# Kernel optimization log

Hardware: AMD Instinct MI355X
Metric: run time of the kernel (lower is better)

The kernel has to match this reference:

```python
import jax, jax.numpy as jnp
import numpy as np

HIDDEN = 768
HEADS = 12
HEAD_DIM = HIDDEN // HEADS
DEPTH = 8
B, S = 4, 512


def setup_inputs() -> dict:
    key = jax.random.key(0)
    ks = jax.random.split(key, 12)
    sc = 0.02
    return {
        "hidden_states": jax.random.normal(ks[0], (B, S, HIDDEN), dtype=jnp.float32),
        "attention_mask": jnp.ones((B, S), dtype=jnp.int32),
        "Wq": jax.random.normal(ks[1], (HIDDEN, HIDDEN), dtype=jnp.float32) * sc,
        "bq": jnp.zeros((HIDDEN,), dtype=jnp.float32),
        "Wk": jax.random.normal(ks[2], (HIDDEN, HIDDEN), dtype=jnp.float32) * sc,
        "bk": jnp.zeros((HIDDEN,), dtype=jnp.float32),
        "Wv": jax.random.normal(ks[3], (HIDDEN, HIDDEN), dtype=jnp.float32) * sc,
        "bv": jnp.zeros((HIDDEN,), dtype=jnp.float32),
        "Wqd": jax.random.normal(ks[4], (HIDDEN * DEPTH, HIDDEN), dtype=jnp.float32) * sc,
        "bqd": jnp.zeros((HIDDEN * DEPTH,), dtype=jnp.float32),
        "Wkd": jax.random.normal(ks[5], (HIDDEN * DEPTH, HIDDEN), dtype=jnp.float32) * sc,
        "bkd": jnp.zeros((HIDDEN * DEPTH,), dtype=jnp.float32),
    }


def reference(hidden_states, attention_mask, Wq, bq, Wk, bk, Wv, bv, Wqd, bqd, Wkd, bkd):
    b, s, _ = hidden_states.shape
    # projections (nn.Linear: x @ W.T + b)
    V = (hidden_states @ Wv.T + bv).reshape(b, s, HEADS, HEAD_DIM).transpose(0, 2, 1, 3)  # [B,H,S,hd]
    Qd = (hidden_states @ Wqd.T + bqd).reshape(b, s, HEADS, HEAD_DIM, DEPTH).transpose(0, 2, 1, 3, 4)  # [B,H,S,hd,D]
    Kd = (hidden_states @ Wkd.T + bkd).reshape(b, s, HEADS, HEAD_DIM, DEPTH).transpose(0, 2, 1, 3, 4)
    # per-depth QK^T scores: [B,H,Sq,Sk,D]
    scores = jnp.einsum('bhqed,bhked->bhqkd', Qd, Kd) / np.sqrt(HEAD_DIM).astype(np.float32)
    # mask broadcasts over the key axis: [B,1,1,S,1]
    mask = attention_mask[:, None, None, :, None]
    scores = jnp.where(mask == 0, jnp.float32(-1e9), scores)
    # softmax over key dim (axis=-2 of [B,H,Sq,Sk,D])
    weights = jax.nn.softmax(scores, axis=3)
    # per-depth AV matmul, stacked on leading depth axis: [D,B,H,S,hd]
    depth_outputs = jnp.einsum('bhqkd,bhke->dbhqe', weights, V)
    return depth_outputs
```

## Files before the change

kernel.cpp:

```cpp
#include <hip/hip_runtime.h>

#define HIDDEN 768
#define HEADS 12
#define HEAD_DIM 64
#define DEPTH 8
#define BB 4
#define SS 512
#define MM (BB * SS)
#define NQD (HIDDEN * DEPTH)

typedef __bf16 bf16x8 __attribute__((ext_vector_type(8)));
typedef float f32x4 __attribute__((ext_vector_type(4)));
typedef float f32x16 __attribute__((ext_vector_type(16)));
typedef unsigned short u16x8 __attribute__((ext_vector_type(8)));

static __device__ __forceinline__ unsigned short f2bf(float f) {
  union { float f; unsigned u; } c; c.f = f;
  unsigned u = c.u;
  u = u + 0x7fffu + ((u >> 16) & 1u);
  return (unsigned short)(u >> 16);
}

static __device__ __forceinline__ unsigned cvt_pk_bf16(float lo, float hi) {
  unsigned r;
  asm("v_cvt_pk_bf16_f32 %0, %1, %2" : "=v"(r) : "v"(lo), "v"(hi));
  return r;
}

static __device__ __forceinline__ void gld16(const void* g, void* l) {
  __builtin_amdgcn_global_load_lds((const __attribute__((address_space(1))) void*)g,
                                   (__attribute__((address_space(3))) void*)l, 16, 0, 0);
}

__global__ void convert2_f32_bf16(const float* __restrict__ s0, unsigned short* __restrict__ d0,
                                  int n4_0, const float* __restrict__ s1,
                                  unsigned short* __restrict__ d1, int n4_1) {
  int i = blockIdx.x * blockDim.x + threadIdx.x;
  const float* src; unsigned short* dst; int j;
  if (i < n4_0) { src = s0; dst = d0; j = i; }
  else { j = i - n4_0; if (j >= n4_1) return; src = s1; dst = d1; }
  float4 v = reinterpret_cast<const float4*>(src)[j];
  ushort4 o;
  o.x = f2bf(v.x); o.y = f2bf(v.y); o.z = f2bf(v.z); o.w = f2bf(v.w);
  reinterpret_cast<ushort4*>(dst)[j] = o;
}

__global__ void convert_w_perm2(const float* __restrict__ s0, const float* __restrict__ s1,
                                unsigned short* __restrict__ dst, int n4each) {
  int i = blockIdx.x * blockDim.x + threadIdx.x;
  const float* src = s0; unsigned short* d = dst; int j = i;
  if (i >= n4each) {
    j = i - n4each;
    if (j >= n4each) return;
    src = s1; d = dst + (size_t)NQD * HIDDEN;
  }
  int row = j / 192;
  int cg  = j - row * 192;
  int nr = (row & ~511) | ((row & 7) << 6) | ((row >> 3) & 63);
  float4 v = reinterpret_cast<const float4*>(src)[j];
  ushort4 o;
  o.x = f2bf(v.x); o.y = f2bf(v.y); o.z = f2bf(v.z); o.w = f2bf(v.w);
  reinterpret_cast<ushort4*>(&d[(size_t)nr * HIDDEN])[cg] = o;
}

__global__ void convert_bias_perm2(const float* __restrict__ s0, const float* __restrict__ s1,
                                   float* __restrict__ dst, int n) {
  int i = blockIdx.x * blockDim.x + threadIdx.x;
  const float* src = s0; float* d = dst; int j = i;
  if (i >= n) {
    j = i - n;
    if (j >= n) return;
    src = s1; d = dst + n;
  }
  int nr = (j & ~511) | ((j & 7) << 6) | ((j >> 3) & 63);
  d[nr] = src[j];
}

__global__ __launch_bounds__(256) void gemm_bt(
    const unsigned short* __restrict__ A, const unsigned short* __restrict__ W,
    const float* __restrict__ bias, unsigned short* __restrict__ out0, int K) {
  __shared__ unsigned short At[2][4096];
  __shared__ unsigned short Bt[2][4096];
  const int tid = threadIdx.x;
  const int nwg = gridDim.x * gridDim.y;
  const int orig = blockIdx.y * gridDim.x + blockIdx.x;
  const int wg = (orig & 7) * (nwg >> 3) + (orig >> 3);
  const int bm = (wg % gridDim.x) * 128;
  const int bn = (wg / gridDim.x) * 128;
  const int wave = tid >> 6, lane = tid & 63;
  const int wm = (wave >> 1) * 64, wn = (wave & 1) * 64;
  const int lg = lane >> 4, lr = lane & 15;
  const int srow = tid >> 2, scol = (tid & 3) * 8;
  f32x4 acc[4][4] = {};
  const unsigned short* aptr = A + (size_t)(bm + srow) * K + scol;
  const unsigned short* wptr = W + (size_t)(bn + srow) * K + scol;

  auto stage = [&](int buf, int k0) {
    gld16(aptr + k0,                  &At[buf][tid * 8]);
    gld16(aptr + (size_t)64 * K + k0, &At[buf][2048 + tid * 8]);
    gld16(wptr + k0,                  &Bt[buf][tid * 8]);
    gld16(wptr + (size_t)64 * K + k0, &Bt[buf][2048 + tid * 8]);
  };

  stage(0, 0);
  __syncthreads();

  int cur = 0;
  for (int k0 = 32; k0 <= K; k0 += 32) {
    if (k0 < K) stage(cur ^ 1, k0);
    bf16x8 af[4], bfr[4];
#pragma unroll
    for (int mi = 0; mi < 4; ++mi)
      af[mi] = *reinterpret_cast<const bf16x8*>(&At[cur][(wm + mi * 16 + lr) * 32 + lg * 8]);
#pragma unroll
    for (int ni = 0; ni < 4; ++ni)
      bfr[ni] = *reinterpret_cast<const bf16x8*>(&Bt[cur][(wn + ni * 16 + lr) * 32 + lg * 8]);
#pragma unroll
    for (int mi = 0; mi < 4; ++mi)
#pragma unroll
      for (int ni = 0; ni < 4; ++ni)
        acc[mi][ni] = __builtin_amdgcn_mfma_f32_16x16x32_bf16(af[mi], bfr[ni], acc[mi][ni], 0, 0, 0);
    __syncthreads();
    cur ^= 1;
  }

#pragma unroll
  for (int mi = 0; mi < 4; ++mi)
#pragma unroll
    for (int ni = 0; ni < 4; ++ni)
#pragma unroll
      for (int i = 0; i < 4; ++i) {
        int m = bm + wm + mi * 16 + lg * 4 + i;
        int n = bn + wn + ni * 16 + lr;
        float v = acc[mi][ni][i] + bias[m];
        size_t addr = ((size_t)((n >> 9) * 12 + (m >> 6)) * 64 + (size_t)(m & 63)) * 512 + (size_t)(n & 511);
        out0[addr] = f2bf(v);
      }
}

__global__ __launch_bounds__(512, 2) void gemm_qk256(
    const unsigned short* __restrict__ A, const unsigned short* __restrict__ W,
    const float* __restrict__ bias, unsigned short* __restrict__ out0,
    unsigned short* __restrict__ out1, int K) {
  __shared__ unsigned short At[2][8192];
  __shared__ unsigned short Bt[2][6144];
  const int tid = threadIdx.x;
  const int nwg = gridDim.x * gridDim.y;
  const int orig = blockIdx.y * gridDim.x + blockIdx.x;
  const int wg = (orig & 7) * (nwg >> 3) + (orig >> 3);
  const int bm = (wg % gridDim.x) * 256;
  const int bn = (wg / gridDim.x) * 192;
  const int wave = tid >> 6, lane = tid & 63;
  const int wr = wave >> 2, wc = wave & 3;
  const int lg = lane >> 4, lr = lane & 15;

  const int rA0 = tid >> 2,           cA0 = (tid & 3) << 3;
  const int rA1 = (tid + 512) >> 2;
  const bool hasB1 = tid < 256;
  const int rB1 = (tid + 512) >> 2;
  const int dA0 = rA0 * 64 + ((cA0 << 1) ^ (((rA0 >> 1) & 3) << 4));
  const int dA1 = rA1 * 64 + ((cA0 << 1) ^ (((rA1 >> 1) & 3) << 4));
  const int dB0 = dA0;
  const int dB1 = rB1 * 64 + ((cA0 << 1) ^ (((rB1 >> 1) & 3) << 4));
  const unsigned short* pA0 = A + (size_t)(bm + rA0) * K + cA0;
  const unsigned short* pA1 = A + (size_t)(bm + rA1) * K + cA0;
  const unsigned short* pB0 = W + (size_t)(bn + rA0) * K + cA0;
  const unsigned short* pB1 = W + (size_t)(bn + rB1) * K + cA0;

  u16x8 a0A = {}, a1A = {}, b0A = {}, b1A = {};
  u16x8 a0B = {}, a1B = {}, b0B = {}, b1B = {};

  auto gloadA = [&](int k0) {
    a0A = *reinterpret_cast<const u16x8*>(pA0 + k0);
    a1A = *reinterpret_cast<const u16x8*>(pA1 + k0);
    b0A = *reinterpret_cast<const u16x8*>(pB0 + k0);
    if (hasB1) b1A = *reinterpret_cast<const u16x8*>(pB1 + k0);
  };
  auto gloadB = [&](int k0) {
    a0B = *reinterpret_cast<const u16x8*>(pA0 + k0);
    a1B = *reinterpret_cast<const u16x8*>(pA1 + k0);
    b0B = *reinterpret_cast<const u16x8*>(pB0 + k0);
    if (hasB1) b1B = *reinterpret_cast<const u16x8*>(pB1 + k0);
  };
  auto lwriteA = [&](int buf) {
    *reinterpret_cast<u16x8*>((char*)At[buf] + dA0) = a0A;
    *reinterpret_cast<u16x8*>((char*)At[buf] + dA1) = a1A;
    *reinterpret_cast<u16x8*>((char*)Bt[buf] + dB0) = b0A;
    if (hasB1) *reinterpret_cast<u16x8*>((char*)Bt[buf] + dB1) = b1A;
  };
  auto lwriteB = [&](int buf) {
    *reinterpret_cast<u16x8*>((char*)At[buf] + dA0) = a0B;
    *reinterpret_cast<u16x8*>((char*)At[buf] + dA1) = a1B;
    *reinterpret_cast<u16x8*>((char*)Bt[buf] + dB0) = b0B;
    if (hasB1) *reinterpret_cast<u16x8*>((char*)Bt[buf] + dB1) = b1B;
  };

  const int rdswz = ((((lr >> 1) & 3) ^ lg) << 4);

  f32x4 acc[8][3] = {};
  auto compute = [&](int buf) {
    bf16x8 af[8], bfr[3];
    const char* abase = (const char*)At[buf];
    const char* bbase = (const char*)Bt[buf];
#pragma unroll
    for (int mi = 0; mi < 8; ++mi) {
      const int row = wr * 128 + mi * 16 + lr;
      af[mi] = *reinterpret_cast<const bf16x8*>(abase + row * 64 + rdswz);
    }
#pragma unroll
    for (int ni = 0; ni < 3; ++ni) {
      const int row = wc * 48 + ni * 16 + lr;
      bfr[ni] = *reinterpret_cast<const bf16x8*>(bbase + row * 64 + rdswz);
    }
#pragma unroll
    for (int mi = 0; mi < 8; ++mi)
#pragma unroll
      for (int ni = 0; ni < 3; ++ni)
        acc[mi][ni] = __builtin_amdgcn_mfma_f32_16x16x32_bf16(af[mi], bfr[ni], acc[mi][ni], 0, 0, 0);
  };

  const int NT = K / 32;
  gloadA(0);
  gloadB(32);
  lwriteA(0);
  __syncthreads();

  for (int tt = 0; tt < NT; tt += 2) {
    if (tt + 2 < NT) gloadA((tt + 2) * 32);
    compute(0);
    if (tt + 1 < NT) lwriteB(1);
    __syncthreads();
    if (tt + 1 < NT) {
      if (tt + 3 < NT) gloadB((tt + 3) * 32);
      compute(1);
      if (tt + 2 < NT) lwriteA(0);
      __syncthreads();
    }
  }

  unsigned short* outp = out0;
  int nbase = 0;
  float scale = 0.125f;
  if (bn >= NQD) { outp = out1; nbase = NQD; scale = 1.0f; }
#pragma unroll
  for (int mi = 0; mi < 8; ++mi)
#pragma unroll
    for (int ni = 0; ni < 3; ++ni)
#pragma unroll
      for (int i = 0; i < 4; ++i) {
        int m = bm + wr * 128 + mi * 16 + lg * 4 + i;
        int n = bn + wc * 48 + ni * 16 + lr;
        float v = (acc[mi][ni][i] + bias[n]) * scale;
        int nr = n - nbase;
        size_t addr = ((size_t)(((m >> 9) * 12 + (nr >> 9)) * 8 + ((nr >> 6) & 7)) * 512 + (size_t)(m & 511)) * 64 + (size_t)(nr & 63);
        outp[addr] = f2bf(v);
      }
}

__global__ __launch_bounds__(256) void attn32(
    const unsigned short* __restrict__ Qd, const unsigned short* __restrict__ Kd,
    const unsigned short* __restrict__ Vt, const int* __restrict__ mask,
    float* __restrict__ out) {
  __shared__ unsigned char KsB[64 * 128];
  __shared__ unsigned char VsB[64 * 128];
  __shared__ float mLds[64];
  __shared__ int mflag;
  const int tid = threadIdx.x;
  const int bid = blockIdx.x;
  const int qt = bid & 3;
  const int inst = bid >> 2;
  const int bh = inst >> 3;
  const int b = bh / 12;
  const int wave = tid >> 6, lane = tid & 63;
  const int l31 = lane & 31, hi = lane >> 5;
  const size_t qkbase = (size_t)inst * (SS * 64);
  const size_t vbase = (size_t)bh * (64 * SS);

  if (tid == 0) mflag = 0;
  __syncthreads();
  {
    int m0 = mask[b * SS + tid], m1 = mask[b * SS + 256 + tid];
    if ((m0 == 0) || (m1 == 0)) mflag = 1;
  }
  __syncthreads();
  const bool hasmask = (mflag != 0);

  const int q0w = qt * 128 + wave * 32;
  bf16x8 aq[4];
  {
    const unsigned short* qrow = Qd + qkbase + (size_t)(q0w + l31) * 64 + 8 * hi;
#pragma unroll
    for (int s = 0; s < 4; ++s)
      aq[s] = *reinterpret_cast<const bf16x8*>(qrow + 16 * s);
  }

  const int sr = tid >> 3;
  const int sc = (tid & 7) * 8;
  const int swz_lo = sr * 128 + ((sc * 2) ^ ((sr & 7) << 4));
  const int swz_hi = (sr + 32) * 128 + ((sc * 2) ^ (((sr + 32) & 7) << 4));

  f32x16 o[2] = {};
  float psum = 0.f;

  u16x8 rk0 = *reinterpret_cast<const u16x8*>(&Kd[qkbase + (size_t)sr * 64 + sc]);
  u16x8 rk1 = *reinterpret_cast<const u16x8*>(&Kd[qkbase + (size_t)(sr + 32) * 64 + sc]);
  u16x8 rv0 = *reinterpret_cast<const u16x8*>(&Vt[vbase + (size_t)sr * SS + sc]);
  u16x8 rv1 = *reinterpret_cast<const u16x8*>(&Vt[vbase + (size_t)(sr + 32) * SS + sc]);

  for (int t = 0; t < SS / 64; ++t) {
    *reinterpret_cast<u16x8*>(KsB + swz_lo) = rk0;
    *reinterpret_cast<u16x8*>(KsB + swz_hi) = rk1;
    *reinterpret_cast<u16x8*>(VsB + swz_lo) = rv0;
    *reinterpret_cast<u16x8*>(VsB + swz_hi) = rv1;
    if (hasmask && tid < 64) mLds[tid] = mask[b * SS + t * 64 + tid] ? 0.f : -1e9f;
    __syncthreads();

    if (t < SS / 64 - 1) {
      const int kn = (t + 1) * 64;
      rk0 = *reinterpret_cast<const u16x8*>(&Kd[qkbase + (size_t)(kn + sr) * 64 + sc]);
      rk1 = *reinterpret_cast<const u16x8*>(&Kd[qkbase + (size_t)(kn + sr + 32) * 64 + sc]);
      rv0 = *reinterpret_cast<const u16x8*>(&Vt[vbase + (size_t)sr * SS + kn + sc]);
      rv1 = *reinterpret_cast<const u16x8*>(&Vt[vbase + (size_t)(sr + 32) * SS + kn + sc]);
    }

    f32x16 st[2];
    __builtin_amdgcn_s_setprio(1);
#pragma unroll
    for (int kh = 0; kh < 2; ++kh) {
      f32x16 acc = {};
      const int row = kh * 32 + l31;
      const int rswz = (row & 7) << 4;
#pragma unroll
      for (int s = 0; s < 4; ++s) {
        bf16x8 ak = *reinterpret_cast<const bf16x8*>(KsB + row * 128 + ((32 * s + 16 * hi) ^ rswz));
        acc = __builtin_amdgcn_mfma_f32_32x32x16_bf16(ak, aq[s], acc, 0, 0, 0);
      }
      st[kh] = acc;
    }
    __builtin_amdgcn_s_setprio(0);

    if (hasmask) {
#pragma unroll
      for (int h = 0; h < 2; ++h)
#pragma unroll
        for (int r = 0; r < 16; ++r)
          st[h][r] += mLds[32 * h + (r & 3) + 8 * (r >> 2) + 4 * hi];
    }

    float pv[2][16];
#pragma unroll
    for (int h = 0; h < 2; ++h)
#pragma unroll
      for (int r = 0; r < 16; ++r) {
        float p = __expf(st[h][r]);
        psum += p;
        pv[h][r] = p;
      }

    __builtin_amdgcn_s_setprio(1);
#pragma unroll
    for (int ks = 0; ks < 4; ++ks) {
      const int h = ks >> 1, rb = 8 * (ks & 1);
      unsigned w0 = cvt_pk_bf16(pv[h][rb + 0], pv[h][rb + 1]);
      unsigned w1 = cvt_pk_bf16(pv[h][rb + 2], pv[h][rb + 3]);
      unsigned w2 = cvt_pk_bf16(pv[h][rb + 4], pv[h][rb + 5]);
      unsigned w3 = cvt_pk_bf16(pv[h][rb + 6], pv[h][rb + 7]);
      asm("v_permlane32_swap_b32 %0, %1" : "+v"(w0), "+v"(w2));
      asm("v_permlane32_swap_b32 %0, %1" : "+v"(w1), "+v"(w3));
      union { unsigned u[4]; bf16x8 v; } pa;
      pa.u[0] = w0; pa.u[1] = w1; pa.u[2] = w2; pa.u[3] = w3;
#pragma unroll
      for (int et = 0; et < 2; ++et) {
        const int vrow = 32 * et + l31;
        bf16x8 bv = *reinterpret_cast<const bf16x8*>(
            VsB + vrow * 128 + ((32 * ks + 16 * hi) ^ ((vrow & 7) << 4)));
        o[et] = __builtin_amdgcn_mfma_f32_32x32x16_bf16(pa.v, bv, o[et], 0, 0, 0);
      }
    }
    __builtin_amdgcn_s_setprio(0);
    __syncthreads();
  }

  psum += __shfl_xor(psum, 32);
  float inv = 1.f / psum;
  float iv[16];
#pragma unroll
  for (int r = 0; r < 16; ++r)
    iv[r] = __shfl(inv, (r & 3) + 8 * (r >> 2) + 4 * hi);

  const int d = inst & 7;
  const int hh = bh % 12;
  const size_t obase = (((size_t)d * BB + b) * HEADS + hh) * (SS * 64);
#pragma unroll
  for (int et = 0; et < 2; ++et)
#pragma unroll
    for (int r = 0; r < 16; ++r) {
      const int qrow = (r & 3) + 8 * (r >> 2) + 4 * hi;
      out[obase + (size_t)(q0w + qrow) * 64 + 32 * et + l31] = o[et][r] * iv[r];
    }
}

extern "C" void kernel_launch(void* const* d_in, const int* in_sizes, int n_in,
                              void* d_out, int out_size, void* d_ws, size_t ws_size,
                              hipStream_t stream) {
  const float* hs  = (const float*)d_in[0];
  const int* mask  = (const int*)d_in[1];
  const float* Wv  = (const float*)d_in[6];
  const float* bv  = (const float*)d_in[7];
  const float* Wqd = (const float*)d_in[8];
  const float* bqd = (const float*)d_in[9];
  const float* Wkd = (const float*)d_in[10];
  const float* bkd = (const float*)d_in[11];

  char* ws = (char*)d_ws;
  unsigned short* A_bf   = (unsigned short*)ws; ws += (size_t)MM * HIDDEN * 2;
  unsigned short* Wv_bf  = (unsigned short*)ws; ws += (size_t)HIDDEN * HIDDEN * 2;
  unsigned short* Wqk_bf = (unsigned short*)ws; ws += (size_t)(2 * NQD) * HIDDEN * 2;
  float*          bqk_p  = (float*)ws;          ws += (size_t)(2 * NQD) * 4;
  unsigned short* Qd     = (unsigned short*)ws; ws += (size_t)MM * NQD * 2;
  unsigned short* Kd     = (unsigned short*)ws; ws += (size_t)MM * NQD * 2;
  unsigned short* Vt     = (unsigned short*)ws; ws += (size_t)MM * HIDDEN * 2;

  {
    int a4 = MM * HIDDEN / 4, b4 = HIDDEN * HIDDEN / 4;
    convert2_f32_bf16<<<(a4 + b4 + 255) / 256, 256, 0, stream>>>(hs, A_bf, a4, Wv, Wv_bf, b4);
  }
  {
    int n4 = NQD * HIDDEN / 4;
    convert_w_perm2<<<(2 * n4 + 255) / 256, 256, 0, stream>>>(Wqd, Wkd, Wqk_bf, n4);
    convert_bias_perm2<<<(2 * NQD + 255) / 256, 256, 0, stream>>>(bqd, bkd, bqk_p, NQD);
  }

  gemm_bt<<<dim3(HIDDEN / 128, MM / 128), 256, 0, stream>>>(
      Wv_bf, A_bf, bv, Vt, HIDDEN);
  gemm_qk256<<<dim3(MM / 256, 2 * NQD / 192), 512, 0, stream>>>(
      A_bf, Wqk_bf, bqk_p, Qd, Kd, HIDDEN);

  attn32<<<BB * HEADS * DEPTH * (SS / 128), 256, 0, stream>>>(Qd, Kd, Vt, mask, (float*)d_out);
}
```

Measured before the change: 132.1 us.

## Split attention key range across two wave groups with LDS reduction

The attention kernel grows from 256 to 512 threads. Two groups of four waves each process half of the key sequence for the same query tile, each with its own K/V LDS buffers. At the end, group 1 writes its partial outputs and row sums to shared memory and group 0 adds them before normalizing and storing. The aim is more parallelism and latency hiding per block, paid for with a shared-memory reduction, extra LDS use and possibly lower occupancy.

```diff
diff --git a/kernel.cpp b/kernel.cpp
--- a/kernel.cpp
+++ b/kernel.cpp
@@ -257,13 +257,12 @@
       }
 }
 
-__global__ __launch_bounds__(256) void attn32(
+__global__ __launch_bounds__(512) void attn32(
     const unsigned short* __restrict__ Qd, const unsigned short* __restrict__ Kd,
     const unsigned short* __restrict__ Vt, const int* __restrict__ mask,
     float* __restrict__ out) {
-  __shared__ unsigned char KsB[64 * 128];
-  __shared__ unsigned char VsB[64 * 128];
-  __shared__ float mLds[64];
+  __shared__ __align__(16) char smem[32768 + 512];
+  __shared__ float psbuf[4][64];
   __shared__ int mflag;
   const int tid = threadIdx.x;
   const int bid = blockIdx.x;
@@ -272,20 +271,21 @@
   const int bh = inst >> 3;
   const int b = bh / 12;
   const int wave = tid >> 6, lane = tid & 63;
+  const int grp = wave >> 2, w4 = wave & 3;
   const int l31 = lane & 31, hi = lane >> 5;
   const size_t qkbase = (size_t)inst * (SS * 64);
   const size_t vbase = (size_t)bh * (64 * SS);
+  unsigned char* KsB = (unsigned char*)smem + grp * 8192;
+  unsigned char* VsB = (unsigned char*)smem + 16384 + grp * 8192;
+  float* mLds = (float*)(smem + 32768) + grp * 64;
 
   if (tid == 0) mflag = 0;
   __syncthreads();
-  {
-    int m0 = mask[b * SS + tid], m1 = mask[b * SS + 256 + tid];
-    if ((m0 == 0) || (m1 == 0)) mflag = 1;
-  }
+  if (mask[b * SS + tid] == 0) mflag = 1;
   __syncthreads();
   const bool hasmask = (mflag != 0);
 
-  const int q0w = qt * 128 + wave * 32;
+  const int q0w = qt * 128 + w4 * 32;
   bf16x8 aq[4];
   {
     const unsigned short* qrow = Qd + qkbase + (size_t)(q0w + l31) * 64 + 8 * hi;
@@ -294,29 +294,31 @@
       aq[s] = *reinterpret_cast<const bf16x8*>(qrow + 16 * s);
   }
 
-  const int sr = tid >> 3;
-  const int sc = (tid & 7) * 8;
+  const int t256 = tid & 255;
+  const int sr = t256 >> 3;
+  const int sc = (t256 & 7) * 8;
   const int swz_lo = sr * 128 + ((sc * 2) ^ ((sr & 7) << 4));
   const int swz_hi = (sr + 32) * 128 + ((sc * 2) ^ (((sr + 32) & 7) << 4));
+  const int kg = grp * 256;
 
   f32x16 o[2] = {};
   float psum = 0.f;
 
-  u16x8 rk0 = *reinterpret_cast<const u16x8*>(&Kd[qkbase + (size_t)sr * 64 + sc]);
-  u16x8 rk1 = *reinterpret_cast<const u16x8*>(&Kd[qkbase + (size_t)(sr + 32) * 64 + sc]);
-  u16x8 rv0 = *reinterpret_cast<const u16x8*>(&Vt[vbase + (size_t)sr * SS + sc]);
-  u16x8 rv1 = *reinterpret_cast<const u16x8*>(&Vt[vbase + (size_t)(sr + 32) * SS + sc]);
-
-  for (int t = 0; t < SS / 64; ++t) {
+  u16x8 rk0 = *reinterpret_cast<const u16x8*>(&Kd[qkbase + (size_t)(kg + sr) * 64 + sc]);
+  u16x8 rk1 = *reinterpret_cast<const u16x8*>(&Kd[qkbase + (size_t)(kg + sr + 32) * 64 + sc]);
+  u16x8 rv0 = *reinterpret_cast<const u16x8*>(&Vt[vbase + (size_t)sr * SS + kg + sc]);
+  u16x8 rv1 = *reinterpret_cast<const u16x8*>(&Vt[vbase + (size_t)(sr + 32) * SS + kg + sc]);
+
+  for (int t = 0; t < 4; ++t) {
     *reinterpret_cast<u16x8*>(KsB + swz_lo) = rk0;
     *reinterpret_cast<u16x8*>(KsB + swz_hi) = rk1;
     *reinterpret_cast<u16x8*>(VsB + swz_lo) = rv0;
     *reinterpret_cast<u16x8*>(VsB + swz_hi) = rv1;
-    if (hasmask && tid < 64) mLds[tid] = mask[b * SS + t * 64 + tid] ? 0.f : -1e9f;
+    if (hasmask && t256 < 64) mLds[t256] = mask[b * SS + kg + t * 64 + t256] ? 0.f : -1e9f;
     __syncthreads();
 
-    if (t < SS / 64 - 1) {
-      const int kn = (t + 1) * 64;
+    if (t < 3) {
+      const int kn = kg + (t + 1) * 64;
       rk0 = *reinterpret_cast<const u16x8*>(&Kd[qkbase + (size_t)(kn + sr) * 64 + sc]);
       rk1 = *reinterpret_cast<const u16x8*>(&Kd[qkbase + (size_t)(kn + sr + 32) * 64 + sc]);
       rv0 = *reinterpret_cast<const u16x8*>(&Vt[vbase + (size_t)sr * SS + kn + sc]);
@@ -381,23 +383,41 @@
     __syncthreads();
   }
 
-  psum += __shfl_xor(psum, 32);
-  float inv = 1.f / psum;
-  float iv[16];
-#pragma unroll
-  for (int r = 0; r < 16; ++r)
-    iv[r] = __shfl(inv, (r & 3) + 8 * (r >> 2) + 4 * hi);
-
-  const int d = inst & 7;
-  const int hh = bh % 12;
-  const size_t obase = (((size_t)d * BB + b) * HEADS + hh) * (SS * 64);
-#pragma unroll
-  for (int et = 0; et < 2; ++et)
-#pragma unroll
-    for (int r = 0; r < 16; ++r) {
-      const int qrow = (r & 3) + 8 * (r >> 2) + 4 * hi;
-      out[obase + (size_t)(q0w + qrow) * 64 + 32 * et + l31] = o[et][r] * iv[r];
-    }
+  float* cbuf = (float*)smem;
+  if (grp == 1) {
+#pragma unroll
+    for (int et = 0; et < 2; ++et)
+#pragma unroll
+      for (int r = 0; r < 16; ++r)
+        cbuf[(et * 16 + r) * 256 + w4 * 64 + lane] = o[et][r];
+    psbuf[w4][lane] = psum;
+  }
+  __syncthreads();
+  if (grp == 0) {
+#pragma unroll
+    for (int et = 0; et < 2; ++et)
+#pragma unroll
+      for (int r = 0; r < 16; ++r)
+        o[et][r] += cbuf[(et * 16 + r) * 256 + w4 * 64 + lane];
+    psum += psbuf[w4][lane];
+    psum += __shfl_xor(psum, 32);
+    float inv = 1.f / psum;
+    float iv[16];
+#pragma unroll
+    for (int r = 0; r < 16; ++r)
+      iv[r] = __shfl(inv, (r & 3) + 8 * (r >> 2) + 4 * hi);
+
+    const int d = inst & 7;
+    const int hh = bh % 12;
+    const size_t obase = (((size_t)d * BB + b) * HEADS + hh) * (SS * 64);
+#pragma unroll
+    for (int et = 0; et < 2; ++et)
+#pragma unroll
+      for (int r = 0; r < 16; ++r) {
+        const int qrow = (r & 3) + 8 * (r >> 2) + 4 * hi;
+        out[obase + (size_t)(q0w + qrow) * 64 + 32 * et + l31] = o[et][r] * iv[r];
+      }
+  }
 }
 
 extern "C" void kernel_launch(void* const* d_in, const int* in_sizes, int n_in,
@@ -436,5 +456,5 @@
   gemm_qk256<<<dim3(MM / 256, 2 * NQD / 192), 512, 0, stream>>>(
       A_bf, Wqk_bf, bqk_p, Qd, Kd, HIDDEN);
 
-  attn32<<<BB * HEADS * DEPTH * (SS / 128), 256, 0, stream>>>(Qd, Kd, Vt, mask, (float*)d_out);
-}
+  attn32<<<BB * HEADS * DEPTH * (SS / 128), 512, 0, stream>>>(Qd, Kd, Vt, mask, (float*)d_out);
+}
```

New measurement: 141.9 us. 7.4% more time.
